# Optimization experiments

Hardware: AMD Instinct MI355X
Metric: run time of the kernel (lower is better)

Reference implementation:

```python
import jax, jax.numpy as jnp
import numpy as np

B, L, E = 64, 256, 512
H = 1024          # hidden_size
M = 2048          # memory_size
HS = 64           # head_size
R = 4             # num_reads
O = 1024          # output_size
CI = E + R * HS   # controller input size = 768
PO = H + R * HS   # pre-output size = 1280
EPS = 1e-5


def _ln(x, g, b):
    mu = jnp.mean(x, axis=-1, keepdims=True)
    var = jnp.mean(jnp.square(x - mu), axis=-1, keepdims=True)
    return (x - mu) * jax.lax.rsqrt(var + EPS) * g + b


def setup_inputs() -> dict:
    key = jax.random.key(0)
    ks = jax.random.split(key, 16)
    s = 0.02
    inp = {
        'x_emb': jax.random.normal(ks[0], (B, L, E), jnp.float32),
        # input LayerNorm
        'ln_in_g': jnp.ones((CI,), jnp.float32), 'ln_in_b': jnp.zeros((CI,), jnp.float32),
        # LSTM (PyTorch gate order i,f,g,o)
        'w_ih': jax.random.normal(ks[1], (4 * H, CI), jnp.float32) * s,
        'w_hh': jax.random.normal(ks[2], (4 * H, H), jnp.float32) * s,
        'b_ih': jnp.zeros((4 * H,), jnp.float32), 'b_hh': jnp.zeros((4 * H,), jnp.float32),
        # controller LayerNorm
        'ln_c_g': jnp.ones((H,), jnp.float32), 'ln_c_b': jnp.zeros((H,), jnp.float32),
        # heads
        'w_rk': jax.random.normal(ks[3], (R * HS, H), jnp.float32) * s, 'b_rk': jnp.zeros((R * HS,), jnp.float32),
        'w_wk': jax.random.normal(ks[4], (HS, H), jnp.float32) * s, 'b_wk': jnp.zeros((HS,), jnp.float32),
        'w_ws': jax.random.normal(ks[5], (1, H), jnp.float32) * s, 'b_ws': jnp.zeros((1,), jnp.float32),
        'w_er': jax.random.normal(ks[6], (HS, H), jnp.float32) * s, 'b_er': jnp.zeros((HS,), jnp.float32),
        'w_ad': jax.random.normal(ks[7], (HS, H), jnp.float32) * s, 'b_ad': jnp.zeros((HS,), jnp.float32),
        # key / memory LayerNorms
        'ln_rk_g': jnp.ones((HS,), jnp.float32), 'ln_rk_b': jnp.zeros((HS,), jnp.float32),
        'ln_wk_g': jnp.ones((HS,), jnp.float32), 'ln_wk_b': jnp.zeros((HS,), jnp.float32),
        'ln_m_g': jnp.ones((HS,), jnp.float32), 'ln_m_b': jnp.zeros((HS,), jnp.float32),
        # pre-output LayerNorm + projection
        'ln_o_g': jnp.ones((PO,), jnp.float32), 'ln_o_b': jnp.zeros((PO,), jnp.float32),
        'w_p': jax.random.normal(ks[8], (O, PO), jnp.float32) * s, 'b_p': jnp.zeros((O,), jnp.float32),
    }
    return inp


def _dnc_forward(x_emb, ln_in_g, ln_in_b, w_ih, w_hh, b_ih, b_hh, ln_c_g, ln_c_b,
                 w_rk, b_rk, w_wk, b_wk, w_ws, b_ws, w_er, b_er, w_ad, b_ad,
                 ln_rk_g, ln_rk_b, ln_wk_g, ln_wk_b, ln_m_g, ln_m_b,
                 ln_o_g, ln_o_b, w_p, b_p):
    Bq = x_emb.shape[0]
    h0 = jnp.zeros((Bq, H), x_emb.dtype)
    c0 = jnp.zeros((Bq, H), x_emb.dtype)
    mem0 = jnp.zeros((Bq, M, HS), x_emb.dtype)
    rv0 = jnp.zeros((Bq, R * HS), x_emb.dtype)

    def step(carry, x_t):
        h, c, mem, rv = carry
        ci = _ln(jnp.concatenate([x_t, rv], axis=-1), ln_in_g, ln_in_b)
        gates = ci @ w_ih.T + b_ih + h @ w_hh.T + b_hh  # [B, 4H]
        i, f, g, o = jnp.split(gates, 4, axis=-1)
        c_new = jax.nn.sigmoid(f) * c + jax.nn.sigmoid(i) * jnp.tanh(g)
        h_new = jax.nn.sigmoid(o) * jnp.tanh(c_new)
        hn = _ln(h_new, ln_c_g, ln_c_b)
        read_keys = (hn @ w_rk.T + b_rk).reshape(Bq, R, HS)
        write_keys = hn @ w_wk.T + b_wk                       # [B, HS]
        write_str = jax.nn.sigmoid(hn @ w_ws.T + b_ws)        # [B, 1]
        erase_vec = jax.nn.sigmoid(hn @ w_er.T + b_er)        # [B, HS]
        add_vec = jnp.tanh(hn @ w_ad.T + b_ad)                # [B, HS]
        # write: content-based attention over normalized memory
        mem_n = _ln(mem, ln_m_g, ln_m_b)
        wk_n = _ln(write_keys, ln_wk_g, ln_wk_b)
        ww = jax.nn.softmax(jnp.einsum('bh,bmh->bm', wk_n, mem_n), axis=1) * write_str  # [B, M]
        mem = mem * (1.0 - ww[:, :, None] * erase_vec[:, None, :]) + ww[:, :, None] * add_vec[:, None, :]
        # read from updated memory
        mem_n2 = _ln(mem, ln_m_g, ln_m_b)
        rk_n = _ln(read_keys, ln_rk_g, ln_rk_b)
        rw = jax.nn.softmax(jnp.einsum('bnh,bmh->bnm', rk_n, mem_n2), axis=2)
        rv_new = jnp.einsum('bnm,bmh->bnh', rw, mem).reshape(Bq, R * HS)
        out = _ln(jnp.concatenate([hn, rv_new], axis=-1), ln_o_g, ln_o_b)
        logits = out @ w_p.T + b_p
        return (h_new, c_new, mem, rv_new), logits

    (hT, cT, memT, _), ys = jax.lax.scan(step, (h0, c0, mem0, rv0), jnp.swapaxes(x_emb, 0, 1))
    outputs = jnp.swapaxes(ys, 0, 1)  # [B, L, O]
    return outputs, memT, (hT[None], cT[None])


def reference(x_emb, ln_in_g, ln_in_b, w_ih, w_hh, b_ih, b_hh, ln_c_g, ln_c_b,
              w_rk, b_rk, w_wk, b_wk, w_ws, b_ws, w_er, b_er, w_ad, b_ad,
              ln_rk_g, ln_rk_b, ln_wk_g, ln_wk_b, ln_m_g, ln_m_b,
              ln_o_g, ln_o_b, w_p, b_p):
    return _dnc_forward(x_emb, ln_in_g, ln_in_b, w_ih, w_hh, b_ih, b_hh, ln_c_g, ln_c_b,
                        w_rk, b_rk, w_wk, b_wk, w_ws, b_ws, w_er, b_er, w_ad, b_ad,
                        ln_rk_g, ln_rk_b, ln_wk_g, ln_wk_b, ln_m_g, ln_m_b,
                        ln_o_g, ln_o_b, w_p, b_p)
```

## Files before the change

kernel.cpp:

```cpp
#include <hip/hip_runtime.h>
#include <math.h>

#define BB 64
#define LL 256
#define EE 512
#define HH 1024
#define MM 2048
#define HSZ 64
#define RR 4
#define CIN 768
#define PO 1280
#define OO 1024
#define EPSF 1e-5f
#define NT 512
#define NB_REQ 256
#define MS 36
#define CSL 512

#define OUT_Y    0
#define OUT_MEM  (BB * LL * OO)
#define OUT_HT   (OUT_MEM + BB * MM * HSZ)
#define OUT_CT   (OUT_HT + BB * HH)

#define WS_RAW   0
#define WS_SW    512
#define WS_SRD   1024
#define WS_BCG   3072
#define WS_PHN   3200
#define WS_RKN   4224
#define WS_WKN   4480
#define WS_ERS   4544
#define WS_ADS   4608
#define WS_WSS   4672
#define WS_PART  5120
#define WS_ROW   5120
#define WS_CIROW 6400
#define WS_GEMM_A  0
#define WS_GEMM_W  2176
#define WS_GEMM_G  10880
#define WS_FLOATS  13056
#define DYN_BYTES ((512*MS + WS_FLOATS) * 4)

struct Params {
  const float *x_emb, *ln_in_g, *ln_in_b, *w_ih, *w_hh, *b_ih, *b_hh;
  const float *ln_c_g, *ln_c_b, *w_rk, *b_rk, *w_wk, *b_wk, *w_ws, *b_ws;
  const float *w_er, *b_er, *w_ad, *b_ad, *ln_rk_g, *ln_rk_b, *ln_wk_g, *ln_wk_b;
  const float *ln_m_g, *ln_m_b, *ln_o_g, *ln_o_b, *w_p, *b_p;
  float *y, *mem, *ht, *ct;
  float *c, *wpart, *rpart, *rvpart;
  unsigned *h16, *ci16, *orow16;
  unsigned short *wih16, *whh16, *wp16, *whd16;
  unsigned *bar;
};

__device__ __forceinline__ float sigm(float x){ return 1.f/(1.f+expf(-x)); }
__device__ __forceinline__ float bl(unsigned u){ return __uint_as_float(u<<16); }
__device__ __forceinline__ float bh(unsigned u){ return __uint_as_float(u & 0xffff0000u); }
__device__ __forceinline__ unsigned pk2(float a, float b){
  unsigned ua = __float_as_uint(a), ub = __float_as_uint(b);
  ua = (ua + 0x7fffu + ((ua>>16)&1u)) >> 16;
  ub = (ub + 0x7fffu + ((ub>>16)&1u)) >> 16;
  return ua | (ub<<16);
}

__device__ __forceinline__ unsigned dloadu(const unsigned* p){
  return __hip_atomic_load(p, __ATOMIC_RELAXED, __HIP_MEMORY_SCOPE_AGENT);
}
__device__ __forceinline__ uint2 dloadu2(const unsigned* p){
  unsigned long long u = __hip_atomic_load((const unsigned long long*)p,
                                           __ATOMIC_RELAXED, __HIP_MEMORY_SCOPE_AGENT);
  uint2 r; r.x = (unsigned)(u & 0xffffffffull); r.y = (unsigned)(u >> 32); return r;
}
__device__ __forceinline__ void dstoreu(unsigned* p, unsigned v){
  __hip_atomic_store(p, v, __ATOMIC_RELAXED, __HIP_MEMORY_SCOPE_AGENT);
}
__device__ __forceinline__ float dloadf(const float* p){
  return __hip_atomic_load(p, __ATOMIC_RELAXED, __HIP_MEMORY_SCOPE_AGENT);
}
__device__ __forceinline__ void dstoref(float* p, float v){
  __hip_atomic_store(p, v, __ATOMIC_RELAXED, __HIP_MEMORY_SCOPE_AGENT);
}

__device__ __forceinline__ void lds_barrier() {
  asm volatile("s_waitcnt lgkmcnt(0)" ::: "memory");
  __builtin_amdgcn_sched_barrier(0);
  __builtin_amdgcn_s_barrier();
  __builtin_amdgcn_sched_barrier(0);
}

__device__ __forceinline__ void gbar(unsigned* bar, unsigned bnum) {
  __syncthreads();
  if (threadIdx.x == 0) {
    asm volatile("s_waitcnt vmcnt(0)" ::: "memory");
    int g = blockIdx.x & 15;
    unsigned a = __hip_atomic_fetch_add(&bar[16 + g*16], 1u,
                    __ATOMIC_RELAXED, __HIP_MEMORY_SCOPE_AGENT) + 1u;
    if (a == bnum * 16u) {
      unsigned r = __hip_atomic_fetch_add(&bar[0], 1u,
                      __ATOMIC_RELAXED, __HIP_MEMORY_SCOPE_AGENT) + 1u;
      if (r == bnum * 16u) {
        #pragma unroll
        for (int i=0;i<16;++i)
          __hip_atomic_fetch_add(&bar[512 + i*16], 1u,
                                 __ATOMIC_RELAXED, __HIP_MEMORY_SCOPE_AGENT);
      }
    }
    while (__hip_atomic_load(&bar[512 + g*16], __ATOMIC_RELAXED,
                             __HIP_MEMORY_SCOPE_AGENT) < bnum) {
      __builtin_amdgcn_s_sleep(8);
    }
    asm volatile("" ::: "memory");
  }
  __syncthreads();
}

__device__ __forceinline__ float bsum(float v, volatile float* red){
  __syncthreads();
  for (int o=32;o>0;o>>=1) v += __shfl_down(v,o,64);
  int w = threadIdx.x>>6;
  if ((threadIdx.x&63)==0) red[w]=v;
  __syncthreads();
  return red[0]+red[1]+red[2]+red[3]+red[4]+red[5]+red[6]+red[7];
}
__device__ __forceinline__ float bmax(float v, volatile float* red){
  __syncthreads();
  for (int o=32;o>0;o>>=1) v = fmaxf(v,__shfl_down(v,o,64));
  int w = threadIdx.x>>6;
  if ((threadIdx.x&63)==0) red[w]=v;
  __syncthreads();
  float a = fmaxf(fmaxf(red[0],red[1]),fmaxf(red[2],red[3]));
  float b = fmaxf(fmaxf(red[4],red[5]),fmaxf(red[6],red[7]));
  return fmaxf(a,b);
}

__device__ __forceinline__ float row_score(const float4* v, const float* wk,
                                           const float* g, const float* bt){
  float sum=0.f;
  #pragma unroll
  for (int i=0;i<16;++i) sum += v[i].x+v[i].y+v[i].z+v[i].w;
  float mu = sum*(1.f/64.f);
  float ssq=0.f;
  #pragma unroll
  for (int i=0;i<16;++i){ float dx=v[i].x-mu,dy=v[i].y-mu,dz=v[i].z-mu,dw=v[i].w-mu;
                          ssq+=dx*dx+dy*dy+dz*dz+dw*dw; }
  float rstd = rsqrtf(ssq*(1.f/64.f)+EPSF);
  float sc=0.f;
  #pragma unroll
  for (int i=0;i<16;++i){ int h=i*4;
    sc += ((v[i].x-mu)*rstd*g[h  ]+bt[h  ])*wk[h  ];
    sc += ((v[i].y-mu)*rstd*g[h+1]+bt[h+1])*wk[h+1];
    sc += ((v[i].z-mu)*rstd*g[h+2]+bt[h+2])*wk[h+2];
    sc += ((v[i].w-mu)*rstd*g[h+3]+bt[h+3])*wk[h+3];
  }
  return sc;
}

__device__ __forceinline__ void load_row_l(const unsigned* rp, float4* rr){
  const uint4* r16 = (const uint4*)rp;
  #pragma unroll
  for (int j=0;j<8;++j){
    uint4 q = r16[j];
    rr[2*j]   = make_float4(bl(q.x),bh(q.x),bl(q.y),bh(q.y));
    rr[2*j+1] = make_float4(bl(q.z),bh(q.z),bl(q.w),bh(q.w));
  }
}
__device__ __forceinline__ void store_row_l(unsigned* rp, const float4* rr){
  uint4* r16 = (uint4*)rp;
  #pragma unroll
  for (int j=0;j<8;++j){
    uint4 q;
    q.x = pk2(rr[2*j].x,   rr[2*j].y);
    q.y = pk2(rr[2*j].z,   rr[2*j].w);
    q.z = pk2(rr[2*j+1].x, rr[2*j+1].y);
    q.w = pk2(rr[2*j+1].z, rr[2*j+1].w);
    r16[j] = q;
  }
}

__device__ void logits_tile(const Params& p, int w, int tid, int tprev, float* ws){
  const unsigned* ob16 = p.orow16 + (size_t)(tprev&1)*BB*(PO/2);
  int cgl = w & 15, bg = w >> 4;
  int sub = tid >> 8, stid = tid & 255;
  int tb = stid >> 4, cq = stid & 15;
  int ar = tb, ac = cq << 2;
  int b0 = bg*16, col0 = cgl*64;
  float (*A_)[68]  = (float(*)[68])(ws + WS_GEMM_A);
  float (*Wt_)[68] = (float(*)[68])(ws + WS_GEMM_W);
  float (*Lc_)[68] = (float(*)[68])(ws + WS_GEMM_G);
  int c0 = cq*4;
  float acc0=0,acc1=0,acc2=0,acc3=0;
  uint2 aPre; uint4 wPre[2];
  const int NIT = 10;
  {
    int k0 = (0*2 + sub)*64;
    aPre = dloadu2(&ob16[((b0+ar)*PO + k0 + ac)>>1]);
    #pragma unroll
    for (int i2=0;i2<2;++i2){
      int li = i2*256 + stid; int ccl = li>>3; int kq = (stid&7)*8;
      wPre[i2] = *(const uint4*)&p.wp16[(size_t)(col0+ccl)*PO + k0 + kq];
    }
  }
  for (int it=0; it<NIT; ++it){
    A_[sub*16+ar][ac]=bl(aPre.x); A_[sub*16+ar][ac+1]=bh(aPre.x);
    A_[sub*16+ar][ac+2]=bl(aPre.y); A_[sub*16+ar][ac+3]=bh(aPre.y);
    #pragma unroll
    for (int i2=0;i2<2;++i2){
      int li = i2*256 + stid; int ccl = li>>3; int kq = (stid&7)*8;
      float f0=bl(wPre[i2].x),f1=bh(wPre[i2].x),f2=bl(wPre[i2].y),f3=bh(wPre[i2].y);
      float f4=bl(wPre[i2].z),f5=bh(wPre[i2].z),f6=bl(wPre[i2].w),f7=bh(wPre[i2].w);
      Wt_[sub*64+kq  ][ccl ^ ((((kq  )>>2)&7)<<2)] = f0;
      Wt_[sub*64+kq+1][ccl ^ ((((kq+1)>>2)&7)<<2)] = f1;
      Wt_[sub*64+kq+2][ccl ^ ((((kq+2)>>2)&7)<<2)] = f2;
      Wt_[sub*64+kq+3][ccl ^ ((((kq+3)>>2)&7)<<2)] = f3;
      Wt_[sub*64+kq+4][ccl ^ ((((kq+4)>>2)&7)<<2)] = f4;
      Wt_[sub*64+kq+5][ccl ^ ((((kq+5)>>2)&7)<<2)] = f5;
      Wt_[sub*64+kq+6][ccl ^ ((((kq+6)>>2)&7)<<2)] = f6;
      Wt_[sub*64+kq+7][ccl ^ ((((kq+7)>>2)&7)<<2)] = f7;
    }
    int nx = (it+1 < NIT) ? it+1 : it;
    {
      int k0 = (nx*2 + sub)*64;
      aPre = dloadu2(&ob16[((b0+ar)*PO + k0 + ac)>>1]);
      #pragma unroll
      for (int i2=0;i2<2;++i2){
        int li = i2*256 + stid; int ccl = li>>3; int kq = (stid&7)*8;
        wPre[i2] = *(const uint4*)&p.wp16[(size_t)(col0+ccl)*PO + k0 + kq];
      }
    }
    lds_barrier();
    #pragma unroll
    for (int kk=0;kk<16;++kk){
      float4 a4 = *(const float4*)&A_[sub*16+tb][kk*4];
      int cs = c0 ^ ((kk&7)<<2);
      float4 w0=*(const float4*)&Wt_[sub*64+kk*4  ][cs];
      float4 w1=*(const float4*)&Wt_[sub*64+kk*4+1][cs];
      float4 w2=*(const float4*)&Wt_[sub*64+kk*4+2][cs];
      float4 w3=*(const float4*)&Wt_[sub*64+kk*4+3][cs];
      acc0+=a4.x*w0.x; acc1+=a4.x*w0.y; acc2+=a4.x*w0.z; acc3+=a4.x*w0.w;
      acc0+=a4.y*w1.x; acc1+=a4.y*w1.y; acc2+=a4.y*w1.z; acc3+=a4.y*w1.w;
      acc0+=a4.z*w2.x; acc1+=a4.z*w2.y; acc2+=a4.z*w2.z; acc3+=a4.z*w2.w;
      acc0+=a4.w*w3.x; acc1+=a4.w*w3.y; acc2+=a4.w*w3.z; acc3+=a4.w*w3.w;
    }
    lds_barrier();
  }
  Lc_[sub*16+tb][c0]=acc0; Lc_[sub*16+tb][c0+1]=acc1;
  Lc_[sub*16+tb][c0+2]=acc2; Lc_[sub*16+tb][c0+3]=acc3;
  __syncthreads();
  if (tid < 256) {
    int tb2 = tid>>4, jl = tid&15;
    int cc0 = jl*4;
    int col = col0 + cc0;
    float4 o;
    o.x = Lc_[tb2][cc0]  +Lc_[16+tb2][cc0]   + p.b_p[col];
    o.y = Lc_[tb2][cc0+1]+Lc_[16+tb2][cc0+1] + p.b_p[col+1];
    o.z = Lc_[tb2][cc0+2]+Lc_[16+tb2][cc0+2] + p.b_p[col+2];
    o.w = Lc_[tb2][cc0+3]+Lc_[16+tb2][cc0+3] + p.b_p[col+3];
    *(float4*)&p.y[(size_t)((b0+tb2)*LL + tprev)*OO + col] = o;
  }
  __syncthreads();
}

__global__ __launch_bounds__(NT, 2) void dnc_all(Params p) {
  extern __shared__ unsigned dyn_lds[];
  unsigned* mrow = dyn_lds;
  float* ws = (float*)(dyn_lds + 512*MS);
  __shared__ float red[8];
  const int blk = blockIdx.x, tid = threadIdx.x;
  const int NB = gridDim.x;
  const int bP = blk >> 2, chP = blk & 3;
  const int wlog = ((bP & 1) << 3) | ((bP >> 1) & 7) | (bP & 48);
  unsigned bnum = 0;

  {
    int gidx = blk*NT + tid, gstr = NB*NT;
    for (int i = gidx; i < (4096*CIN)/2; i += gstr){
      float2 f = *(const float2*)&p.w_ih[2*(size_t)i];
      dstoreu((unsigned*)p.wih16 + i, pk2(f.x, f.y));
    }
    for (int i = gidx; i < (4096*HH)/2; i += gstr){
      float2 f = *(const float2*)&p.w_hh[2*(size_t)i];
      dstoreu((unsigned*)p.whh16 + i, pk2(f.x, f.y));
    }
    for (int i = gidx; i < (OO*PO)/2; i += gstr){
      float2 f = *(const float2*)&p.w_p[2*(size_t)i];
      dstoreu((unsigned*)p.wp16 + i, pk2(f.x, f.y));
    }
    for (int i = gidx; i < 449*512; i += gstr){
      int gr = i >> 9, kp = (i & 511)*2;
      const float* wrow = (gr<256)? p.w_rk + (size_t)gr*HH :
                          (gr<320)? p.w_wk + (size_t)(gr-256)*HH :
                          (gr==320)? p.w_ws :
                          (gr<385)? p.w_er + (size_t)(gr-321)*HH :
                                    p.w_ad + (size_t)(gr-385)*HH;
      dstoreu((unsigned*)p.whd16 + i, pk2(wrow[kp], wrow[kp+1]));
    }
    for (int i = tid; i < 512*MS; i += NT) mrow[i] = 0u;
    for (int i = gidx; i < (BB*HH)/2; i += gstr) dstoreu(&p.h16[i], 0u);
    if (blk < BB) {
      int b = blk;
      for (int i = tid; i < CIN; i += NT)
        ws[i] = (i < EE) ? p.x_emb[(size_t)(b*LL)*EE + i] : 0.f;
      __syncthreads();
      float s = 0.f;
      for (int i = tid; i < CIN; i += NT) s += ws[i];
      float mu = bsum(s, red) * (1.f/CIN);
      float ss = 0.f;
      for (int i = tid; i < CIN; i += NT) { float d = ws[i]-mu; ss += d*d; }
      float rstd = rsqrtf(bsum(ss, red)*(1.f/CIN) + EPSF);
      for (int i2 = tid; i2 < CIN/2; i2 += NT){
        float v0 = (ws[2*i2]-mu)*rstd*p.ln_in_g[2*i2] + p.ln_in_b[2*i2];
        float v1 = (ws[2*i2+1]-mu)*rstd*p.ln_in_g[2*i2+1] + p.ln_in_b[2*i2+1];
        dstoreu(&p.ci16[b*(CIN/2)+i2], pk2(v0, v1));
      }
    }
  }
  gbar(p.bar, ++bnum);

  for (int t = 0; t < LL; ++t) {
    const unsigned* hprev16 = p.h16 + (t & 1) * ((BB*HH)>>1);
    unsigned* hnew16 = p.h16 + ((t+1) & 1) * ((BB*HH)>>1);

    for (int w = blk; w < 256; w += NB) {
      int cgp = (w & 7) | (((w >> 3) & 7) << 3);
      int bg = w >> 6;
      int sub = tid >> 8, stid = tid & 255;
      int tb = stid >> 4, cq = stid & 15;
      int ar = tb, ac = cq << 2;
      int b0 = bg*16, j0 = cgp*16;
      float (*A_)[68]  = (float(*)[68])(ws + WS_GEMM_A);
      float (*Wt_)[68] = (float(*)[68])(ws + WS_GEMM_W);
      float (*Gv_)[68] = (float(*)[68])(ws + WS_GEMM_G);
      int c0 = cq*4;
      float acc0=0,acc1=0,acc2=0,acc3=0;
      uint2 aPre; uint4 wPre[2];
      const int NIT = 14;
      {
        int k0 = sub*64;
        aPre = dloadu2(&p.ci16[((b0+ar)*CIN + k0 + ac)>>1]);
        #pragma unroll
        for (int i2=0;i2<2;++i2){
          int li = i2*256 + stid; int ccl = li>>3; int kq = (stid&7)*8;
          int gate = ccl>>4, jl = ccl&15;
          wPre[i2] = *(const uint4*)&p.wih16[(size_t)(gate*HH + j0 + jl)*CIN + k0 + kq];
        }
      }
      for (int it=0; it<NIT; ++it){
        A_[sub*16+ar][ac]=bl(aPre.x); A_[sub*16+ar][ac+1]=bh(aPre.x);
        A_[sub*16+ar][ac+2]=bl(aPre.y); A_[sub*16+ar][ac+3]=bh(aPre.y);
        #pragma unroll
        for (int i2=0;i2<2;++i2){
          int li = i2*256 + stid; int ccl = li>>3; int kq = (stid&7)*8;
          float f0=bl(wPre[i2].x),f1=bh(wPre[i2].x),f2=bl(wPre[i2].y),f3=bh(wPre[i2].y);
          float f4=bl(wPre[i2].z),f5=bh(wPre[i2].z),f6=bl(wPre[i2].w),f7=bh(wPre[i2].w);
          Wt_[sub*64+kq  ][ccl ^ ((((kq  )>>2)&7)<<2)] = f0;
          Wt_[sub*64+kq+1][ccl ^ ((((kq+1)>>2)&7)<<2)] = f1;
          Wt_[sub*64+kq+2][ccl ^ ((((kq+2)>>2)&7)<<2)] = f2;
          Wt_[sub*64+kq+3][ccl ^ ((((kq+3)>>2)&7)<<2)] = f3;
          Wt_[sub*64+kq+4][ccl ^ ((((kq+4)>>2)&7)<<2)] = f4;
          Wt_[sub*64+kq+5][ccl ^ ((((kq+5)>>2)&7)<<2)] = f5;
          Wt_[sub*64+kq+6][ccl ^ ((((kq+6)>>2)&7)<<2)] = f6;
          Wt_[sub*64+kq+7][ccl ^ ((((kq+7)>>2)&7)<<2)] = f7;
        }
        int nx = (it+1 < NIT) ? it+1 : it;
        {
          const unsigned* As16; const unsigned short* Ws16; int K, k0;
          if (nx < 6){ As16 = p.ci16;  Ws16 = p.wih16; K = CIN; k0 = (nx*2 + sub)*64; }
          else       { As16 = hprev16; Ws16 = p.whh16; K = HH;  k0 = ((nx-6)*2 + sub)*64; }
          aPre = dloadu2(&As16[((b0+ar)*K + k0 + ac)>>1]);
          #pragma unroll
          for (int i2=0;i2<2;++i2){
            int li = i2*256 + stid; int ccl = li>>3; int kq = (stid&7)*8;
            int gate = ccl>>4, jl = ccl&15;
            wPre[i2] = *(const uint4*)&Ws16[(size_t)(gate*HH + j0 + jl)*K + k0 + kq];
          }
        }
        lds_barrier();
        #pragma unroll
        for (int kk=0;kk<16;++kk){
          float4 a4 = *(const float4*)&A_[sub*16+tb][kk*4];
          int cs = c0 ^ ((kk&7)<<2);
          float4 w0=*(const float4*)&Wt_[sub*64+kk*4  ][cs];
          float4 w1=*(const float4*)&Wt_[sub*64+kk*4+1][cs];
          float4 w2=*(const float4*)&Wt_[sub*64+kk*4+2][cs];
          float4 w3=*(const float4*)&Wt_[sub*64+kk*4+3][cs];
          acc0+=a4.x*w0.x; acc1+=a4.x*w0.y; acc2+=a4.x*w0.z; acc3+=a4.x*w0.w;
          acc0+=a4.y*w1.x; acc1+=a4.y*w1.y; acc2+=a4.y*w1.z; acc3+=a4.y*w1.w;
          acc0+=a4.z*w2.x; acc1+=a4.z*w2.y; acc2+=a4.z*w2.z; acc3+=a4.z*w2.w;
          acc0+=a4.w*w3.x; acc1+=a4.w*w3.y; acc2+=a4.w*w3.z; acc3+=a4.w*w3.w;
        }
        lds_barrier();
      }
      Gv_[sub*16+tb][c0]=acc0; Gv_[sub*16+tb][c0+1]=acc1;
      Gv_[sub*16+tb][c0+2]=acc2; Gv_[sub*16+tb][c0+3]=acc3;
      __syncthreads();
      if (tid < 256) {
        int tb2 = tid>>4, jl = tid&15;
        int r0 = 0*HH + j0 + jl, r1 = 1*HH + j0 + jl, r2 = 2*HH + j0 + jl, r3 = 3*HH + j0 + jl;
        float gi = Gv_[tb2][jl]    + Gv_[16+tb2][jl]    + p.b_ih[r0]+p.b_hh[r0];
        float gf = Gv_[tb2][16+jl] + Gv_[16+tb2][16+jl] + p.b_ih[r1]+p.b_hh[r1];
        float gg = Gv_[tb2][32+jl] + Gv_[16+tb2][32+jl] + p.b_ih[r2]+p.b_hh[r2];
        float go = Gv_[tb2][48+jl] + Gv_[16+tb2][48+jl] + p.b_ih[r3]+p.b_hh[r3];
        int idx3 = (b0+tb2)*HH + j0 + jl;
        float cold = (t==0) ? 0.f : p.c[idx3];
        float cn = sigm(gf)*cold + sigm(gi)*tanhf(gg);
        float hv = sigm(go)*tanhf(cn);
        p.c[idx3] = cn;
        float hvn = __shfl_down(hv, 1, 64);
        if ((tid & 1) == 0)
          dstoreu(&hnew16[idx3>>1], pk2(hv, hvn));
        if (t == LL-1) { p.ht[idx3] = hv; p.ct[idx3] = cn; }
      }
      __syncthreads();
    }
    gbar(p.bar, ++bnum);

    {
      float* bcg = ws + WS_BCG;
      float* raw = ws + WS_RAW;
      float* pHn = ws + WS_PHN;
      if (tid < 64) { bcg[tid] = p.ln_m_g[tid]; bcg[64+tid] = p.ln_m_b[tid]; }
      unsigned hu = dloadu(&hnew16[(bP*HH>>1) + tid]);
      float hx = bl(hu), hy = bh(hu);
      float s = bsum(hx + hy, red);
      float mu = s * (1.f/HH);
      float d0 = hx-mu, d1 = hy-mu;
      float ssq = bsum(d0*d0 + d1*d1, red);
      float rstd = rsqrtf(ssq*(1.f/HH)+EPSF);
      pHn[tid*2]   = d0*rstd*p.ln_c_g[tid*2]   + p.ln_c_b[tid*2];
      pHn[tid*2+1] = d1*rstd*p.ln_c_g[tid*2+1] + p.ln_c_b[tid*2+1];
      __syncthreads();
      if (tid < 449) {
        int gr = tid;
        float bias;
        if (gr < 256)      bias = p.b_rk[gr];
        else if (gr < 320) bias = p.b_wk[gr-256];
        else if (gr == 320)bias = p.b_ws[0];
        else if (gr < 385) bias = p.b_er[gr-321];
        else               bias = p.b_ad[gr-385];
        const unsigned short* wr16 = p.whd16 + (size_t)gr*HH;
        float acc = bias;
        #pragma unroll 4
        for (int k=0;k<HH;k+=8){
          uint4 q = *(const uint4*)&wr16[k];
          acc += bl(q.x)*pHn[k  ] + bh(q.x)*pHn[k+1] + bl(q.y)*pHn[k+2] + bh(q.y)*pHn[k+3]
               + bl(q.z)*pHn[k+4] + bh(q.z)*pHn[k+5] + bl(q.w)*pHn[k+6] + bh(q.w)*pHn[k+7];
        }
        raw[tid] = acc;
      }
      __syncthreads();
      if (tid < 256) {
        int l = tid & 63;
        float v = raw[tid];
        float sv=v; for(int o=32;o>0;o>>=1) sv += __shfl_xor(sv,o,64);
        float m2 = sv*(1.f/64.f);
        float d = v-m2; float sq=d*d;
        for(int o=32;o>0;o>>=1) sq += __shfl_xor(sq,o,64);
        float rs = rsqrtf(sq*(1.f/64.f)+EPSF);
        ws[WS_RKN + tid] = d*rs*p.ln_rk_g[l] + p.ln_rk_b[l];
      } else if (tid < 320) {
        int l = tid - 256;
        float v = raw[256+l];
        float sv=v; for(int o=32;o>0;o>>=1) sv += __shfl_xor(sv,o,64);
        float m2 = sv*(1.f/64.f);
        float d=v-m2; float sq=d*d;
        for(int o=32;o>0;o>>=1) sq += __shfl_xor(sq,o,64);
        float rs = rsqrtf(sq*(1.f/64.f)+EPSF);
        ws[WS_WKN + l] = d*rs*p.ln_wk_g[l] + p.ln_wk_b[l];
      } else if (tid < 384) {
        int l = tid - 320; ws[WS_ERS + l] = sigm(raw[321+l]);
      } else if (tid < 448) {
        int l = tid - 384; ws[WS_ADS + l] = tanhf(raw[385+l]);
      } else if (tid == 448) {
        ws[WS_WSS] = sigm(raw[320]);
      }
      __syncthreads();
      float4 rr[16];
      load_row_l(mrow + tid*MS, rr);
      float sc = row_score(rr, ws+WS_WKN, bcg, bcg+64);
      ws[WS_SW + tid] = sc;
      float mx = bmax(sc, red);
      float se = bsum(expf(sc-mx), red);
      if (tid==0){ dstoref(&p.wpart[(bP*4+chP)*2], mx); dstoref(&p.wpart[(bP*4+chP)*2+1], se); }
    }
    gbar(p.bar, ++bnum);

    {
      float* bcg = ws + WS_BCG;
      float* srd = ws + WS_SRD;
      float* pRkn = ws + WS_RKN;
      float* pErs = ws + WS_ERS;
      float* pAds = ws + WS_ADS;
      float gmx = -3.4e38f, gsum = 0.f;
      #pragma unroll
      for (int cc=0; cc<4; ++cc) gmx = fmaxf(gmx, dloadf(&p.wpart[(bP*4+cc)*2]));
      #pragma unroll
      for (int cc=0; cc<4; ++cc)
        gsum += dloadf(&p.wpart[(bP*4+cc)*2+1]) * expf(dloadf(&p.wpart[(bP*4+cc)*2]) - gmx);
      float wstr = ws[WS_WSS];
      float ww = expf(ws[WS_SW + tid] - gmx)/gsum * wstr;
      unsigned* rp = mrow + tid*MS;
      float4 rr[16];
      load_row_l(rp, rr);
      #pragma unroll
      for (int i=0;i<16;++i){ int h=i*4;
        rr[i].x = rr[i].x*(1.f-ww*pErs[h  ]) + ww*pAds[h  ];
        rr[i].y = rr[i].y*(1.f-ww*pErs[h+1]) + ww*pAds[h+1];
        rr[i].z = rr[i].z*(1.f-ww*pErs[h+2]) + ww*pAds[h+2];
        rr[i].w = rr[i].w*(1.f-ww*pErs[h+3]) + ww*pAds[h+3];
      }
      store_row_l(rp, rr);
      float sum=0.f;
      #pragma unroll
      for (int i=0;i<16;++i) sum += rr[i].x+rr[i].y+rr[i].z+rr[i].w;
      float mu = sum*(1.f/64.f);
      float ssq=0.f;
      #pragma unroll
      for (int i=0;i<16;++i){ float dx=rr[i].x-mu,dy=rr[i].y-mu,dz=rr[i].z-mu,dw=rr[i].w-mu;
                              ssq+=dx*dx+dy*dy+dz*dz+dw*dw; }
      float rstd = rsqrtf(ssq*(1.f/64.f)+EPSF);
      float sN[4] = {0.f,0.f,0.f,0.f};
      #pragma unroll
      for (int i=0;i<16;++i){ int h=i*4;
        float n0=(rr[i].x-mu)*rstd*bcg[h  ]+bcg[64+h  ];
        float n1=(rr[i].y-mu)*rstd*bcg[h+1]+bcg[64+h+1];
        float n2=(rr[i].z-mu)*rstd*bcg[h+2]+bcg[64+h+2];
        float n3=(rr[i].w-mu)*rstd*bcg[h+3]+bcg[64+h+3];
        sN[0] += n0*pRkn[h    ]+n1*pRkn[h+1    ]+n2*pRkn[h+2    ]+n3*pRkn[h+3    ];
        sN[1] += n0*pRkn[64+h ]+n1*pRkn[64+h+1 ]+n2*pRkn[64+h+2 ]+n3*pRkn[64+h+3 ];
        sN[2] += n0*pRkn[128+h]+n1*pRkn[128+h+1]+n2*pRkn[128+h+2]+n3*pRkn[128+h+3];
        sN[3] += n0*pRkn[192+h]+n1*pRkn[192+h+1]+n2*pRkn[192+h+2]+n3*pRkn[192+h+3];
      }
      #pragma unroll
      for (int n=0;n<RR;++n){
        float mxn = bmax(sN[n], red);
        float sen = bsum(expf(sN[n]-mxn), red);
        srd[n*512 + tid] = expf(sN[n]-mxn);
        if (tid==0){
          dstoref(&p.rpart[(bP*4+chP)*8 + n*2], mxn);
          dstoref(&p.rpart[(bP*4+chP)*8 + n*2+1], sen);
        }
      }
      __syncthreads();
      int hs2 = (tid & 31) * 2, wg = tid >> 5;
      float a00=0,a01=0,a10=0,a11=0,a20=0,a21=0,a30=0,a31=0;
      for (int ml = wg; ml < 512; ml += 16){
        unsigned u = mrow[ml*MS + (hs2>>1)];
        float vlo = bl(u), vhi = bh(u);
        float w0 = srd[ml], w1 = srd[512+ml], w2 = srd[1024+ml], w3 = srd[1536+ml];
        a00 += w0*vlo; a01 += w0*vhi;
        a10 += w1*vlo; a11 += w1*vhi;
        a20 += w2*vlo; a21 += w2*vhi;
        a30 += w3*vlo; a31 += w3*vhi;
      }
      __syncthreads();
      float* part = ws + WS_PART;
      part[(0*16+wg)*64 + hs2] = a00; part[(0*16+wg)*64 + hs2+1] = a01;
      part[(1*16+wg)*64 + hs2] = a10; part[(1*16+wg)*64 + hs2+1] = a11;
      part[(2*16+wg)*64 + hs2] = a20; part[(2*16+wg)*64 + hs2+1] = a21;
      part[(3*16+wg)*64 + hs2] = a30; part[(3*16+wg)*64 + hs2+1] = a31;
      __syncthreads();
      if (tid < 256) {
        int n2 = tid>>6, h2 = tid&63;
        float v = 0.f;
        #pragma unroll
        for (int g2=0; g2<16; ++g2) v += part[(n2*16+g2)*64 + h2];
        dstoref(&p.rvpart[((bP*4+chP)*4 + n2)*64 + h2], v);
      }
    }
    gbar(p.bar, ++bnum);

    if (chP == 0) {
      int b = bP;
      float* row   = ws + WS_ROW;
      float* cirow = ws + WS_CIROW;
      float* pHn   = ws + WS_PHN;
      if (tid < 256) {
        int n = tid>>6, h2 = tid&63;
        float gmxn = -3.4e38f;
        #pragma unroll
        for (int cc=0; cc<4; ++cc) gmxn = fmaxf(gmxn, dloadf(&p.rpart[(b*4+cc)*8 + n*2]));
        float den=0.f, num=0.f;
        #pragma unroll
        for (int cc=0; cc<4; ++cc){
          float e = expf(dloadf(&p.rpart[(b*4+cc)*8 + n*2]) - gmxn);
          den += dloadf(&p.rpart[(b*4+cc)*8 + n*2+1]) * e;
          num += dloadf(&p.rvpart[((b*4+cc)*4 + n)*64 + h2]) * e;
        }
        row[HH + tid] = num/den;
      }
      for (int i=tid;i<HH;i+=NT) row[i] = pHn[i];
      __syncthreads();
      float s=0.f; for (int i=tid;i<PO;i+=NT) s+=row[i];
      float mu = bsum(s,red)*(1.f/PO);
      float ss=0.f; for (int i=tid;i<PO;i+=NT){ float d=row[i]-mu; ss+=d*d; }
      float rstd = rsqrtf(bsum(ss,red)*(1.f/PO)+EPSF);
      unsigned* ob16 = p.orow16 + (size_t)(t&1)*BB*(PO/2);
      for (int i2=tid; i2<PO/2; i2+=NT){
        float v0 = (row[2*i2]-mu)*rstd*p.ln_o_g[2*i2]+p.ln_o_b[2*i2];
        float v1 = (row[2*i2+1]-mu)*rstd*p.ln_o_g[2*i2+1]+p.ln_o_b[2*i2+1];
        dstoreu(&ob16[b*(PO/2)+i2], pk2(v0, v1));
      }
      if (t+1 < LL) {
        for (int i=tid;i<CIN;i+=NT)
          cirow[i] = (i<EE)? p.x_emb[(size_t)(b*LL+t+1)*EE+i] : row[HH+(i-EE)];
        __syncthreads();
        float s2=0.f; for (int i=tid;i<CIN;i+=NT) s2+=cirow[i];
        float mu2 = bsum(s2,red)*(1.f/CIN);
        float ss2=0.f; for (int i=tid;i<CIN;i+=NT){ float d=cirow[i]-mu2; ss2+=d*d; }
        float rstd2 = rsqrtf(bsum(ss2,red)*(1.f/CIN)+EPSF);
        for (int i2=tid; i2<CIN/2; i2+=NT){
          float v0 = (cirow[2*i2]-mu2)*rstd2*p.ln_in_g[2*i2]+p.ln_in_b[2*i2];
          float v1 = (cirow[2*i2+1]-mu2)*rstd2*p.ln_in_g[2*i2+1]+p.ln_in_b[2*i2+1];
          dstoreu(&p.ci16[b*(CIN/2)+i2], pk2(v0, v1));
        }
      }
    } else if (chP == 1 && t > 0) {
      logits_tile(p, wlog, tid, t-1, ws);
    }
    gbar(p.bar, ++bnum);
  }

  {
    float* dst = p.mem + ((size_t)bP*MM + chP*CSL)*HSZ;
    int ml = tid;
    const uint4* src = (const uint4*)(mrow + ml*MS);
    float4* d4 = (float4*)(dst + (size_t)ml*HSZ);
    #pragma unroll
    for (int j=0;j<8;++j){
      uint4 q = src[j];
      d4[2*j]   = make_float4(bl(q.x),bh(q.x),bl(q.y),bh(q.y));
      d4[2*j+1] = make_float4(bl(q.z),bh(q.z),bl(q.w),bh(q.w));
    }
  }
  if (chP == 1) logits_tile(p, wlog, tid, LL-1, ws);
}

extern "C" void kernel_launch(void* const* d_in, const int* in_sizes, int n_in,
                              void* d_out, int out_size, void* d_ws, size_t ws_size,
                              hipStream_t stream) {
  Params prm;
  prm.x_emb  = (const float*)d_in[0];
  prm.ln_in_g= (const float*)d_in[1];
  prm.ln_in_b= (const float*)d_in[2];
  prm.w_ih   = (const float*)d_in[3];
  prm.w_hh   = (const float*)d_in[4];
  prm.b_ih   = (const float*)d_in[5];
  prm.b_hh   = (const float*)d_in[6];
  prm.ln_c_g = (const float*)d_in[7];
  prm.ln_c_b = (const float*)d_in[8];
  prm.w_rk   = (const float*)d_in[9];
  prm.b_rk   = (const float*)d_in[10];
  prm.w_wk   = (const float*)d_in[11];
  prm.b_wk   = (const float*)d_in[12];
  prm.w_ws   = (const float*)d_in[13];
  prm.b_ws   = (const float*)d_in[14];
  prm.w_er   = (const float*)d_in[15];
  prm.b_er   = (const float*)d_in[16];
  prm.w_ad   = (const float*)d_in[17];
  prm.b_ad   = (const float*)d_in[18];
  prm.ln_rk_g= (const float*)d_in[19];
  prm.ln_rk_b= (const float*)d_in[20];
  prm.ln_wk_g= (const float*)d_in[21];
  prm.ln_wk_b= (const float*)d_in[22];
  prm.ln_m_g = (const float*)d_in[23];
  prm.ln_m_b = (const float*)d_in[24];
  prm.ln_o_g = (const float*)d_in[25];
  prm.ln_o_b = (const float*)d_in[26];
  prm.w_p    = (const float*)d_in[27];
  prm.b_p    = (const float*)d_in[28];

  float* out = (float*)d_out;
  prm.y   = out + OUT_Y;
  prm.mem = out + OUT_MEM;
  prm.ht  = out + OUT_HT;
  prm.ct  = out + OUT_CT;

  prm.bar = (unsigned*)d_ws;
  hipMemsetAsync(d_ws, 0, 4096, stream);

  float* ws = (float*)((char*)d_ws + 4096);
  size_t o = 0;
  prm.c      = ws + o; o += BB*HH;
  prm.h16    = (unsigned*)(ws + o); o += BB*HH;
  prm.ci16   = (unsigned*)(ws + o); o += (BB*CIN)/2;
  prm.orow16 = (unsigned*)(ws + o); o += BB*PO;
  prm.wpart  = ws + o; o += 256*2;
  prm.rpart  = ws + o; o += 256*8;
  prm.rvpart = ws + o; o += 256*4*64;
  prm.wih16  = (unsigned short*)(ws + o); o += (4096*CIN)/2;
  prm.whh16  = (unsigned short*)(ws + o); o += (4096*HH)/2;
  prm.wp16   = (unsigned short*)(ws + o); o += (OO*PO)/2;
  prm.whd16  = (unsigned short*)(ws + o); o += (449*HH)/2 + 64;

  hipFuncSetAttribute((const void*)dnc_all,
                      hipFuncAttributeMaxDynamicSharedMemorySize, DYN_BYTES);

  dnc_all<<<dim3(NB_REQ), dim3(NT), DYN_BYTES, stream>>>(prm);
}
```

Baseline: 31.11 ms.

## Split head projection GEMV across four blocks per batch with global barrier

The 449-row head projection per batch row was previously computed redundantly or by a single block with one thread per row. It is now split across the four blocks assigned to each batch row (113 rows each), with four threads per row each summing a quarter of K and combining via shuffles. Results go to a global buffer, then an extra grid barrier lets each block reload the full raw vector. This cuts per-block GEMV latency in the serial recurrent step, at the cost of one more grid-wide barrier per timestep.

```diff
diff --git a/kernel.cpp b/kernel.cpp
--- a/kernel.cpp
+++ b/kernel.cpp
@@ -47,7 +47,7 @@
   const float *w_er, *b_er, *w_ad, *b_ad, *ln_rk_g, *ln_rk_b, *ln_wk_g, *ln_wk_b;
   const float *ln_m_g, *ln_m_b, *ln_o_g, *ln_o_b, *w_p, *b_p;
   float *y, *mem, *ht, *ct;
-  float *c, *wpart, *rpart, *rvpart;
+  float *c, *wpart, *rpart, *rvpart, *rawbuf;
   unsigned *h16, *ci16, *orow16;
   unsigned short *wih16, *whh16, *wp16, *whd16;
   unsigned *bar;
@@ -415,10 +415,7 @@
     gbar(p.bar, ++bnum);
 
     {
-      float* bcg = ws + WS_BCG;
-      float* raw = ws + WS_RAW;
       float* pHn = ws + WS_PHN;
-      if (tid < 64) { bcg[tid] = p.ln_m_g[tid]; bcg[64+tid] = p.ln_m_b[tid]; }
       unsigned hu = dloadu(&hnew16[(bP*HH>>1) + tid]);
       float hx = bl(hu), hy = bh(hu);
       float s = bsum(hx + hy, red);
@@ -429,24 +426,36 @@
       pHn[tid*2]   = d0*rstd*p.ln_c_g[tid*2]   + p.ln_c_b[tid*2];
       pHn[tid*2+1] = d1*rstd*p.ln_c_g[tid*2+1] + p.ln_c_b[tid*2+1];
       __syncthreads();
-      if (tid < 449) {
-        int gr = tid;
-        float bias;
-        if (gr < 256)      bias = p.b_rk[gr];
-        else if (gr < 320) bias = p.b_wk[gr-256];
-        else if (gr == 320)bias = p.b_ws[0];
-        else if (gr < 385) bias = p.b_er[gr-321];
-        else               bias = p.b_ad[gr-385];
+      int lr = tid >> 2, q = tid & 3;
+      int base = chP*113;
+      int cnt = (chP<3) ? 113 : 110;
+      if (lr < cnt) {
+        int gr = base + lr;
         const unsigned short* wr16 = p.whd16 + (size_t)gr*HH;
-        float acc = bias;
+        float acc = 0.f;
+        int k0 = q*256;
         #pragma unroll 4
-        for (int k=0;k<HH;k+=8){
-          uint4 q = *(const uint4*)&wr16[k];
-          acc += bl(q.x)*pHn[k  ] + bh(q.x)*pHn[k+1] + bl(q.y)*pHn[k+2] + bh(q.y)*pHn[k+3]
-               + bl(q.z)*pHn[k+4] + bh(q.z)*pHn[k+5] + bl(q.w)*pHn[k+6] + bh(q.w)*pHn[k+7];
-        }
-        raw[tid] = acc;
-      }
+        for (int k=k0; k<k0+256; k+=8){
+          uint4 qd = *(const uint4*)&wr16[k];
+          acc += bl(qd.x)*pHn[k  ] + bh(qd.x)*pHn[k+1] + bl(qd.y)*pHn[k+2] + bh(qd.y)*pHn[k+3]
+               + bl(qd.z)*pHn[k+4] + bh(qd.z)*pHn[k+5] + bl(qd.w)*pHn[k+6] + bh(qd.w)*pHn[k+7];
+        }
+        acc += __shfl_down(acc, 1, 64);
+        acc += __shfl_down(acc, 2, 64);
+        if (q == 0) {
+          float bias = (gr<256)? p.b_rk[gr] : (gr<320)? p.b_wk[gr-256] :
+                       (gr==320)? p.b_ws[0] : (gr<385)? p.b_er[gr-321] : p.b_ad[gr-385];
+          dstoref(&p.rawbuf[(size_t)bP*452 + gr], acc + bias);
+        }
+      }
+    }
+    gbar(p.bar, ++bnum);
+
+    {
+      float* bcg = ws + WS_BCG;
+      float* raw = ws + WS_RAW;
+      if (tid < 64) { bcg[tid] = p.ln_m_g[tid]; bcg[64+tid] = p.ln_m_b[tid]; }
+      if (tid < 449) raw[tid] = dloadf(&p.rawbuf[(size_t)bP*452 + tid]);
       __syncthreads();
       if (tid < 256) {
         int l = tid & 63;
@@ -687,6 +696,7 @@
   prm.wpart  = ws + o; o += 256*2;
   prm.rpart  = ws + o; o += 256*8;
   prm.rvpart = ws + o; o += 256*4*64;
+  prm.rawbuf = ws + o; o += BB*452;
   prm.wih16  = (unsigned short*)(ws + o); o += (4096*CIN)/2;
   prm.whh16  = (unsigned short*)(ws + o); o += (4096*HH)/2;
   prm.wp16   = (unsigned short*)(ws + o); o += (OO*PO)/2;
```

New measurement: 27.22 ms. -12.5%, faster.
